# Performance work log

Hardware: AMD Instinct MI355X
Metric: run time of the kernel (lower is better)

The kernel has to match this reference:

```python
import jax, jax.numpy as jnp
import numpy as np

N = 100000      # number of nodes
E = 1600000     # number of (directed) edges, avg degree 16
DIN = 128       # in_features
DOUT = 32       # out_features
SLOPE = 0.2     # leaky relu negative slope


def setup_inputs() -> dict:
    key = jax.random.key(0)
    k1, k2, k3, k4, k5, k6 = jax.random.split(key, 6)
    x = jax.random.normal(k1, (N, DIN), dtype=jnp.float32)
    edge_index = jax.random.randint(k2, (2, E), 0, N, dtype=jnp.int32)
    # W1 (shared with W2 and used as the feature-update matrix W, 'source' mode)
    W1_w = jax.random.normal(k3, (DOUT, DIN), dtype=jnp.float32) / np.float32(np.sqrt(DIN))
    W1_b = jax.random.normal(k4, (DOUT,), dtype=jnp.float32) * 0.01
    a1_w = jax.random.normal(k5, (DOUT,), dtype=jnp.float32) / np.float32(np.sqrt(DOUT))
    a2_w = jax.random.normal(k6, (DOUT,), dtype=jnp.float32) / np.float32(np.sqrt(DOUT))
    return {"x": x, "edge_index": edge_index, "W1_w": W1_w, "W1_b": W1_b,
            "a1_w": a1_w, "a2_w": a2_w}


def reference(x, edge_index, W1_w, W1_b, a1_w, a2_w):
    n = x.shape[0]
    # append self-loops, as in _sparse_attention
    loops = jnp.arange(n, dtype=edge_index.dtype)
    src = jnp.concatenate([edge_index[0], loops])   # rows  (softmax segments)
    dst = jnp.concatenate([edge_index[1], loops])   # cols
    # h = W1(x) (linear, with bias); W2 = W1 (weight sharing), W = W2 ('source')
    h = x @ W1_w.T + W1_b                           # [N, DOUT]
    z = jax.nn.leaky_relu(h, SLOPE)                 # x1 == x2 under weight sharing
    s1 = z @ a1_w                                   # [N] per-node src score
    s2 = z @ a2_w                                   # [N] per-node dst score
    logits = s1[src] + s2[dst]                      # [E+N] per-edge attention logit
    # row-wise (dim=1) sparse softmax == segment softmax over src
    m = jax.ops.segment_max(logits, src, num_segments=n)
    ex = jnp.exp(logits - m[src])
    denom = jax.ops.segment_sum(ex, src, num_segments=n)
    alpha = ex / denom[src]                         # normalized attention per edge
    # sparse-dense matmul: out[i] = sum_{(i,j)} alpha_ij * h[j]
    return jax.ops.segment_sum(alpha[:, None] * h[dst], src, num_segments=n)
```

## Files before the change

kernel.cpp:

```cpp
#include <hip/hip_runtime.h>
#include <hip/hip_fp16.h>

#define DIN 128
#define DOUT 32
#define SLOPE 0.2f

#define BSHIFT 7
#define BNODES 128
#define NBS    1024
#define CAP    3072
#define SRTCAP (CAP + 384)
#define TILE   4096
#define EPB    (TILE / 256)
#define TPW    4

typedef short s16x8 __attribute__((ext_vector_type(8)));
typedef float f32x4 __attribute__((ext_vector_type(4)));

__device__ __forceinline__ short f2bf(float f) {
    unsigned u = __float_as_uint(f);
    return (short)((u + 0x7fffu + ((u >> 16) & 1u)) >> 16);
}
__device__ __forceinline__ float bf2f(short s) {
    return __uint_as_float(((unsigned)(unsigned short)s) << 16);
}

__device__ __forceinline__ void linear_role(
    int wid, int ntiles, int lane, int N,
    const float* __restrict__ x, const float* __restrict__ W,
    const float* __restrict__ b, const float* __restrict__ a2,
    __half* __restrict__ g16, float* __restrict__ es2)
{
    if (wid * TPW >= ntiles) return;
    int m = lane & 15, oct = lane >> 4;

    s16x8 bh[2][4], bl[2][4];
    #pragma unroll
    for (int t = 0; t < 2; ++t) {
        const float* wrow = W + (long)(t * 16 + m) * DIN + oct * 8;
        #pragma unroll
        for (int kc = 0; kc < 4; ++kc) {
            float4 w0 = *(const float4*)(wrow + kc * 32);
            float4 w1 = *(const float4*)(wrow + kc * 32 + 4);
            float wf[8] = {w0.x, w0.y, w0.z, w0.w, w1.x, w1.y, w1.z, w1.w};
            #pragma unroll
            for (int j = 0; j < 8; ++j) {
                short hh = f2bf(wf[j]);
                bh[t][kc][j] = hh;
                bl[t][kc][j] = f2bf(wf[j] - bf2f(hh));
            }
        }
    }

    int c0 = m, c1 = 16 + m;
    float b0 = b[c0], b1 = b[c1], A0 = a2[c0], A1 = a2[c1];

    float4 cxa[4];
    {
        long lrow = (long)(wid * TPW) * 16 + m; if (lrow > N - 1) lrow = N - 1;
        const float* xrow = x + lrow * DIN + oct * 8;
        #pragma unroll
        for (int kc = 0; kc < 2; ++kc) {
            cxa[2 * kc]     = *(const float4*)(xrow + kc * 32);
            cxa[2 * kc + 1] = *(const float4*)(xrow + kc * 32 + 4);
        }
    }

    #pragma unroll 1
    for (int g = 0; g < TPW; ++g) {
        int tile = wid * TPW + g;
        if (tile >= ntiles) break;
        long rowbase = (long)tile * 16;
        long lrow = rowbase + m; if (lrow > N - 1) lrow = N - 1;
        const float* xrow = x + lrow * DIN + oct * 8;

        float4 cxb[4];
        #pragma unroll
        for (int kc = 0; kc < 2; ++kc) {
            cxb[2 * kc]     = *(const float4*)(xrow + (kc + 2) * 32);
            cxb[2 * kc + 1] = *(const float4*)(xrow + (kc + 2) * 32 + 4);
        }

        bool hasnext = (g + 1 < TPW) && (tile + 1 < ntiles);
        float4 nxa[4];
        if (hasnext) {
            long nrow = rowbase + 16 + m; if (nrow > N - 1) nrow = N - 1;
            const float* nx = x + nrow * DIN + oct * 8;
            #pragma unroll
            for (int kc = 0; kc < 2; ++kc) {
                nxa[2 * kc]     = *(const float4*)(nx + kc * 32);
                nxa[2 * kc + 1] = *(const float4*)(nx + kc * 32 + 4);
            }
        }

        f32x4 acc0 = {0.f, 0.f, 0.f, 0.f}, acc1 = {0.f, 0.f, 0.f, 0.f};
        #pragma unroll
        for (int kc = 0; kc < 4; ++kc) {
            float4 x0 = (kc < 2) ? cxa[2 * kc]     : cxb[2 * (kc - 2)];
            float4 x1 = (kc < 2) ? cxa[2 * kc + 1] : cxb[2 * (kc - 2) + 1];
            float xf[8] = {x0.x, x0.y, x0.z, x0.w, x1.x, x1.y, x1.z, x1.w};
            s16x8 ah, al;
            #pragma unroll
            for (int j = 0; j < 8; ++j) {
                short hh = f2bf(xf[j]);
                ah[j] = hh;
                al[j] = f2bf(xf[j] - bf2f(hh));
            }
            acc0 = __builtin_amdgcn_mfma_f32_16x16x32_bf16(al, bh[0][kc], acc0, 0, 0, 0);
            acc0 = __builtin_amdgcn_mfma_f32_16x16x32_bf16(ah, bl[0][kc], acc0, 0, 0, 0);
            acc0 = __builtin_amdgcn_mfma_f32_16x16x32_bf16(ah, bh[0][kc], acc0, 0, 0, 0);
            acc1 = __builtin_amdgcn_mfma_f32_16x16x32_bf16(al, bh[1][kc], acc1, 0, 0, 0);
            acc1 = __builtin_amdgcn_mfma_f32_16x16x32_bf16(ah, bl[1][kc], acc1, 0, 0, 0);
            acc1 = __builtin_amdgcn_mfma_f32_16x16x32_bf16(ah, bh[1][kc], acc1, 0, 0, 0);
        }

        float hv0[4], hv1[4], sp[4];
        #pragma unroll
        for (int i = 0; i < 4; ++i) {
            hv0[i] = acc0[i] + b0;
            hv1[i] = acc1[i] + b1;
            float z0 = hv0[i] > 0.f ? hv0[i] : SLOPE * hv0[i];
            float z1 = hv1[i] > 0.f ? hv1[i] : SLOPE * hv1[i];
            sp[i] = z0 * A0 + z1 * A1;
        }
        #pragma unroll
        for (int off = 1; off <= 8; off <<= 1) {
            #pragma unroll
            for (int i = 0; i < 4; ++i) sp[i] += __shfl_xor(sp[i], off, 64);
        }
        #pragma unroll
        for (int i = 0; i < 4; ++i) {
            long r = rowbase + oct * 4 + i;
            if (r >= N) continue;
            float ev = __expf(sp[i]);
            g16[r * DOUT + c0] = __float2half(ev * hv0[i]);
            g16[r * DOUT + c1] = __float2half(ev * hv1[i]);
            if (m == 0) es2[r] = ev;
        }
        if (hasnext) {
            #pragma unroll
            for (int i = 0; i < 4; ++i) cxa[i] = nxa[i];
        }
    }
}

__global__ __launch_bounds__(256) void gat_fused(
    const float* __restrict__ x, const float* __restrict__ W,
    const float* __restrict__ b, const float* __restrict__ a2,
    const int* __restrict__ src, const int* __restrict__ dst,
    __half* __restrict__ g16, float* __restrict__ es2,
    unsigned* __restrict__ ebuf, int* __restrict__ boffT,
    int N, int E, int ntiles, int nbin, int nbinp)
{
    if ((int)blockIdx.x >= nbin) {
        int wave = threadIdx.x >> 6;
        int wid = (blockIdx.x - nbin) * 4 + wave;
        linear_role(wid, ntiles, threadIdx.x & 63, N, x, W, b, a2, g16, es2);
        return;
    }
    __shared__ int cnt[NBS];
    __shared__ int offs[NBS];
    __shared__ int wsum[4], wbase[4];
    int tid = threadIdx.x;
    long tstart = (long)blockIdx.x * TILE;

    for (int i = tid; i < NBS; i += 256) cnt[i] = 0;
    __syncthreads();

    unsigned rec[EPB];
    int      bq[EPB];
    #pragma unroll
    for (int it = 0; it < EPB; ++it) {
        long e = tstart + it * 256 + tid;
        int s = (e < E) ? src[e] : -1;
        int d = (e < E) ? dst[e] : 0;
        if (s >= 0) {
            int bk = s >> BSHIFT;
            int rv = atomicAdd(&cnt[bk], 1);
            rec[it] = ((unsigned)(s & (BNODES - 1)) << 17) | (unsigned)d;
            bq[it] = (rv < 511) ? ((bk << 9) | rv) : -1;
        } else bq[it] = -1;
    }
    __syncthreads();

    int t4 = tid << 2;
    int c0 = cnt[t4], c1 = cnt[t4 + 1], c2 = cnt[t4 + 2], c3 = cnt[t4 + 3];
    int s4 = c0 + c1 + c2 + c3;
    int v = s4;
    #pragma unroll
    for (int off = 1; off < 64; off <<= 1) {
        int t = __shfl_up(v, off, 64);
        if ((tid & 63) >= off) v += t;
    }
    if ((tid & 63) == 63) wsum[tid >> 6] = v;
    __syncthreads();
    if (tid == 0) {
        int a = 0;
        #pragma unroll
        for (int w = 0; w < 4; ++w) { wbase[w] = a; a += wsum[w]; }
    }
    __syncthreads();
    int base = wbase[tid >> 6] + (v - s4);
    offs[t4]     = base;
    offs[t4 + 1] = base + c0;
    offs[t4 + 2] = base + c0 + c1;
    offs[t4 + 3] = base + c0 + c1 + c2;
    __syncthreads();

    int NBv = (N + BNODES - 1) >> BSHIFT;
    for (int i = tid; i <= NBv; i += 256)
        boffT[(size_t)i * nbinp + blockIdx.x] = offs[i];

    #pragma unroll
    for (int it = 0; it < EPB; ++it) {
        int q = bq[it];
        if (q >= 0) {
            int pos = offs[q >> 9] + (q & 511);
            ebuf[tstart + pos] = rec[it];
        }
    }
}

__global__ __launch_bounds__(512) void gat_aggregate(
    const __half* __restrict__ g16, const float* __restrict__ es2,
    const unsigned* __restrict__ ebuf, const int* __restrict__ boffT,
    float* __restrict__ out, int N, int nbin, int nbinp)
{
    __shared__ unsigned srt[SRTCAP];
    __shared__ unsigned srca[CAP];
    __shared__ int cnt[BNODES];
    __shared__ int basep[BNODES];
    __shared__ int pos2[BNODES];
    __shared__ int wsum[8], wbase[8], totsh;
    int tid = threadIdx.x;

    int nwg = gridDim.x;
    int xcd = blockIdx.x & 7;
    int q = nwg >> 3, rr = nwg & 7;
    int bk = (xcd < rr ? xcd * (q + 1) : rr * (q + 1) + (xcd - rr) * q)
           + ((int)blockIdx.x >> 3);

    if (tid < BNODES) { cnt[tid] = 0; pos2[tid] = 0; }

    int rstart = 0, rlen = 0;
    if (tid < nbin) {
        rstart = boffT[(size_t)bk * nbinp + tid];
        rlen   = boffT[(size_t)(bk + 1) * nbinp + tid] - rstart;
    }
    int v = rlen;
    #pragma unroll
    for (int off = 1; off < 64; off <<= 1) {
        int t = __shfl_up(v, off, 64);
        if ((tid & 63) >= off) v += t;
    }
    if ((tid & 63) == 63) wsum[tid >> 6] = v;
    __syncthreads();
    if (tid == 0) {
        int a = 0;
        #pragma unroll
        for (int w = 0; w < 8; ++w) { wbase[w] = a; a += wsum[w]; }
        totsh = a;
    }
    __syncthreads();
    int dest = wbase[tid >> 6] + (v - rlen);
    int lim = CAP - dest; if (lim < 0) lim = 0;
    if (rlen > lim) rlen = lim;
    {
        unsigned abase = (unsigned)tid * TILE + (unsigned)rstart;
        for (int j = 0; j < rlen; ++j)
            srca[dest + j] = abase + (unsigned)j;
    }
    __syncthreads();
    int cntb = totsh; if (cntb > CAP) cntb = CAP;

    unsigned held[6];
    #pragma unroll
    for (int k = 0; k < 6; ++k) {
        int r = tid + (k << 9);
        held[k] = 0xFFFFFFFFu;
        if (r < cntb) held[k] = ebuf[(size_t)srca[r]];
    }
    #pragma unroll
    for (int k = 0; k < 6; ++k) {
        unsigned u = held[k];
        if (u != 0xFFFFFFFFu) atomicAdd(&cnt[u >> 17], 1);
    }
    __syncthreads();

    if (tid < 64) {
        int a = cnt[2 * tid], b2 = cnt[2 * tid + 1];
        int pa = (a + 3) & ~3, pb = (b2 + 3) & ~3;
        int s = pa + pb;
        int vv = s;
        #pragma unroll
        for (int off = 1; off < 64; off <<= 1) {
            int t = __shfl_up(vv, off, 64);
            if (tid >= off) vv += t;
        }
        int excl = vv - s;
        basep[2 * tid]     = excl;
        basep[2 * tid + 1] = excl + pa;
    }
    __syncthreads();

    #pragma unroll
    for (int k = 0; k < 6; ++k) {
        unsigned u = held[k];
        if (u != 0xFFFFFFFFu) {
            int sl = (int)(u >> 17);
            int p = basep[sl] + atomicAdd(&pos2[sl], 1);
            srt[p] = u & 0x1FFFFu;
        }
    }
    __syncthreads();

    int unit = tid >> 5, col = tid & 31;
    int lane64 = tid & 63;
    for (int sl = unit; sl < BNODES; sl += 16) {
        long node = (long)bk * BNODES + sl;
        if (node >= N) break;
        float acc = __half2float(g16[node * DOUT + col]);
        float selfe = es2[node];
        float dpart = 0.f;
        int e = basep[sl], e_end = basep[sl] + cnt[sl];

        while (e + 8 <= e_end) {
            uint4 q0 = *(const uint4*)&srt[e];
            uint4 q1 = *(const uint4*)&srt[e + 4];
            float evp = 0.f;
            if (col < 8) evp = es2[srt[e + col]];
            int dn[8] = {(int)q0.x, (int)q0.y, (int)q0.z, (int)q0.w,
                         (int)q1.x, (int)q1.y, (int)q1.z, (int)q1.w};
            unsigned short gv[8];
            #pragma unroll
            for (int j = 0; j < 8; ++j)
                gv[j] = *(const unsigned short*)&g16[(long)dn[j] * DOUT + col];
            dpart += evp;
            #pragma unroll
            for (int j = 0; j < 8; ++j)
                acc += __half2float(*(const __half*)&gv[j]);
            e += 8;
        }
        while (e + 4 <= e_end) {
            uint4 q0 = *(const uint4*)&srt[e];
            float evp = 0.f;
            if (col < 4) evp = es2[srt[e + col]];
            int dn[4] = {(int)q0.x, (int)q0.y, (int)q0.z, (int)q0.w};
            unsigned short gv[4];
            #pragma unroll
            for (int j = 0; j < 4; ++j)
                gv[j] = *(const unsigned short*)&g16[(long)dn[j] * DOUT + col];
            dpart += evp;
            #pragma unroll
            for (int j = 0; j < 4; ++j)
                acc += __half2float(*(const __half*)&gv[j]);
            e += 4;
        }
        for (; e < e_end; ++e) {
            int dn = (int)srt[e];
            acc += __half2float(g16[(long)dn * DOUT + col]);
            if (col == 0) dpart += es2[dn];
        }
        #pragma unroll
        for (int off = 1; off < 8; off <<= 1)
            dpart += __shfl_xor(dpart, off, 64);
        float dtot = __shfl(dpart, lane64 & 32, 64);
        out[node * DOUT + col] = acc / (selfe + dtot);
    }
}

extern "C" void kernel_launch(void* const* d_in, const int* in_sizes, int n_in,
                              void* d_out, int out_size, void* d_ws, size_t ws_size,
                              hipStream_t stream)
{
    const float* x  = (const float*)d_in[0];
    const int*   ei = (const int*)d_in[1];
    const float* W  = (const float*)d_in[2];
    const float* b  = (const float*)d_in[3];
    const float* a2 = (const float*)d_in[5];
    float* out = (float*)d_out;

    int N = in_sizes[0] / DIN;
    int E = in_sizes[1] / 2;
    const int* src = ei;
    const int* dst = ei + E;

    int NB = (N + BNODES - 1) >> BSHIFT;
    int nbin = (E + TILE - 1) / TILE;
    int nbinp = (nbin + 7) & ~7;

    char* ws = (char*)d_ws;
    __half*   g16   = (__half*)ws;  ws += (size_t)N * DOUT * sizeof(__half);
    float*    es2   = (float*)ws;   ws += (size_t)N * sizeof(float);
    int*      boffT = (int*)ws;     ws += (size_t)(NB + 1) * nbinp * sizeof(int);
    unsigned* ebuf  = (unsigned*)ws; ws += (size_t)nbin * TILE * sizeof(unsigned);

    int ntiles = (N + 15) / 16;
    int nwaves = (ntiles + TPW - 1) / TPW;
    int nlin   = (nwaves + 3) / 4;

    gat_fused    <<<nbin + nlin, 256, 0, stream>>>(x, W, b, a2, src, dst,
                                                   g16, es2, ebuf, boffT,
                                                   N, E, ntiles, nbin, nbinp);
    gat_aggregate<<<NB, 512, 0, stream>>>(g16, es2, ebuf, boffT, out, N,
                                          nbin, nbinp);
}
```

Baseline: 155.1 us.

## Stage split bf16 weights in LDS and give each linear wave one tile

Linear-role blocks now convert W into bf16 hi/lo halves once per block and store them in a swizzled 16KB shared buffer, so waves no longer convert W in registers themselves. Each wave processes a single 16-row tile instead of four, which removes the x prefetch pipeline and roughly quadruples the number of linear blocks. Binning blocks now reuse the same shared buffer for their counters. This adds a block-wide conversion and barrier for every small block, and the larger shared allocation applies to binning blocks too, which may reduce occupancy.

```diff
diff --git a/kernel.cpp b/kernel.cpp
--- a/kernel.cpp
+++ b/kernel.cpp
@@ -12,7 +12,8 @@
 #define SRTCAP (CAP + 384)
 #define TILE   4096
 #define EPB    (TILE / 256)
-#define TPW    4
+
+#define FSMEM  16384
 
 typedef short s16x8 __attribute__((ext_vector_type(8)));
 typedef float f32x4 __attribute__((ext_vector_type(4)));
@@ -25,122 +26,77 @@
     return __uint_as_float(((unsigned)(unsigned short)s) << 16);
 }
 
-__device__ __forceinline__ void linear_role(
-    int wid, int ntiles, int lane, int N,
-    const float* __restrict__ x, const float* __restrict__ W,
+__device__ __forceinline__ void linear_tile(
+    int tile, int ntiles, int lane, int N,
+    const unsigned short* __restrict__ Whi, const unsigned short* __restrict__ Wlo,
+    const float* __restrict__ x,
     const float* __restrict__ b, const float* __restrict__ a2,
     __half* __restrict__ g16, float* __restrict__ es2)
 {
-    if (wid * TPW >= ntiles) return;
+    if (tile >= ntiles) return;
     int m = lane & 15, oct = lane >> 4;
 
     s16x8 bh[2][4], bl[2][4];
     #pragma unroll
     for (int t = 0; t < 2; ++t) {
-        const float* wrow = W + (long)(t * 16 + m) * DIN + oct * 8;
+        int row = t * 16 + m;
         #pragma unroll
         for (int kc = 0; kc < 4; ++kc) {
-            float4 w0 = *(const float4*)(wrow + kc * 32);
-            float4 w1 = *(const float4*)(wrow + kc * 32 + 4);
-            float wf[8] = {w0.x, w0.y, w0.z, w0.w, w1.x, w1.y, w1.z, w1.w};
-            #pragma unroll
-            for (int j = 0; j < 8; ++j) {
-                short hh = f2bf(wf[j]);
-                bh[t][kc][j] = hh;
-                bl[t][kc][j] = f2bf(wf[j] - bf2f(hh));
-            }
+            int sch = (kc * 4 + oct) ^ m;
+            bh[t][kc] = *(const s16x8*)((const char*)Whi + row * 256 + sch * 16);
+            bl[t][kc] = *(const s16x8*)((const char*)Wlo + row * 256 + sch * 16);
         }
     }
 
     int c0 = m, c1 = 16 + m;
     float b0 = b[c0], b1 = b[c1], A0 = a2[c0], A1 = a2[c1];
 
-    float4 cxa[4];
-    {
-        long lrow = (long)(wid * TPW) * 16 + m; if (lrow > N - 1) lrow = N - 1;
-        const float* xrow = x + lrow * DIN + oct * 8;
-        #pragma unroll
-        for (int kc = 0; kc < 2; ++kc) {
-            cxa[2 * kc]     = *(const float4*)(xrow + kc * 32);
-            cxa[2 * kc + 1] = *(const float4*)(xrow + kc * 32 + 4);
-        }
-    }
-
-    #pragma unroll 1
-    for (int g = 0; g < TPW; ++g) {
-        int tile = wid * TPW + g;
-        if (tile >= ntiles) break;
-        long rowbase = (long)tile * 16;
-        long lrow = rowbase + m; if (lrow > N - 1) lrow = N - 1;
-        const float* xrow = x + lrow * DIN + oct * 8;
-
-        float4 cxb[4];
-        #pragma unroll
-        for (int kc = 0; kc < 2; ++kc) {
-            cxb[2 * kc]     = *(const float4*)(xrow + (kc + 2) * 32);
-            cxb[2 * kc + 1] = *(const float4*)(xrow + (kc + 2) * 32 + 4);
-        }
-
-        bool hasnext = (g + 1 < TPW) && (tile + 1 < ntiles);
-        float4 nxa[4];
-        if (hasnext) {
-            long nrow = rowbase + 16 + m; if (nrow > N - 1) nrow = N - 1;
-            const float* nx = x + nrow * DIN + oct * 8;
-            #pragma unroll
-            for (int kc = 0; kc < 2; ++kc) {
-                nxa[2 * kc]     = *(const float4*)(nx + kc * 32);
-                nxa[2 * kc + 1] = *(const float4*)(nx + kc * 32 + 4);
-            }
-        }
-
-        f32x4 acc0 = {0.f, 0.f, 0.f, 0.f}, acc1 = {0.f, 0.f, 0.f, 0.f};
-        #pragma unroll
-        for (int kc = 0; kc < 4; ++kc) {
-            float4 x0 = (kc < 2) ? cxa[2 * kc]     : cxb[2 * (kc - 2)];
-            float4 x1 = (kc < 2) ? cxa[2 * kc + 1] : cxb[2 * (kc - 2) + 1];
-            float xf[8] = {x0.x, x0.y, x0.z, x0.w, x1.x, x1.y, x1.z, x1.w};
-            s16x8 ah, al;
-            #pragma unroll
-            for (int j = 0; j < 8; ++j) {
-                short hh = f2bf(xf[j]);
-                ah[j] = hh;
-                al[j] = f2bf(xf[j] - bf2f(hh));
-            }
-            acc0 = __builtin_amdgcn_mfma_f32_16x16x32_bf16(al, bh[0][kc], acc0, 0, 0, 0);
-            acc0 = __builtin_amdgcn_mfma_f32_16x16x32_bf16(ah, bl[0][kc], acc0, 0, 0, 0);
-            acc0 = __builtin_amdgcn_mfma_f32_16x16x32_bf16(ah, bh[0][kc], acc0, 0, 0, 0);
-            acc1 = __builtin_amdgcn_mfma_f32_16x16x32_bf16(al, bh[1][kc], acc1, 0, 0, 0);
-            acc1 = __builtin_amdgcn_mfma_f32_16x16x32_bf16(ah, bl[1][kc], acc1, 0, 0, 0);
-            acc1 = __builtin_amdgcn_mfma_f32_16x16x32_bf16(ah, bh[1][kc], acc1, 0, 0, 0);
-        }
-
-        float hv0[4], hv1[4], sp[4];
-        #pragma unroll
-        for (int i = 0; i < 4; ++i) {
-            hv0[i] = acc0[i] + b0;
-            hv1[i] = acc1[i] + b1;
-            float z0 = hv0[i] > 0.f ? hv0[i] : SLOPE * hv0[i];
-            float z1 = hv1[i] > 0.f ? hv1[i] : SLOPE * hv1[i];
-            sp[i] = z0 * A0 + z1 * A1;
-        }
-        #pragma unroll
-        for (int off = 1; off <= 8; off <<= 1) {
-            #pragma unroll
-            for (int i = 0; i < 4; ++i) sp[i] += __shfl_xor(sp[i], off, 64);
-        }
-        #pragma unroll
-        for (int i = 0; i < 4; ++i) {
-            long r = rowbase + oct * 4 + i;
-            if (r >= N) continue;
-            float ev = __expf(sp[i]);
-            g16[r * DOUT + c0] = __float2half(ev * hv0[i]);
-            g16[r * DOUT + c1] = __float2half(ev * hv1[i]);
-            if (m == 0) es2[r] = ev;
-        }
-        if (hasnext) {
-            #pragma unroll
-            for (int i = 0; i < 4; ++i) cxa[i] = nxa[i];
-        }
+    long rowbase = (long)tile * 16;
+    long lrow = rowbase + m; if (lrow > N - 1) lrow = N - 1;
+    const float* xrow = x + lrow * DIN + oct * 8;
+    f32x4 acc0 = {0.f, 0.f, 0.f, 0.f}, acc1 = {0.f, 0.f, 0.f, 0.f};
+    #pragma unroll
+    for (int kc = 0; kc < 4; ++kc) {
+        float4 x0 = *(const float4*)(xrow + kc * 32);
+        float4 x1 = *(const float4*)(xrow + kc * 32 + 4);
+        float xf[8] = {x0.x, x0.y, x0.z, x0.w, x1.x, x1.y, x1.z, x1.w};
+        s16x8 ah, al;
+        #pragma unroll
+        for (int j = 0; j < 8; ++j) {
+            short hh = f2bf(xf[j]);
+            ah[j] = hh;
+            al[j] = f2bf(xf[j] - bf2f(hh));
+        }
+        acc0 = __builtin_amdgcn_mfma_f32_16x16x32_bf16(al, bh[0][kc], acc0, 0, 0, 0);
+        acc0 = __builtin_amdgcn_mfma_f32_16x16x32_bf16(ah, bl[0][kc], acc0, 0, 0, 0);
+        acc0 = __builtin_amdgcn_mfma_f32_16x16x32_bf16(ah, bh[0][kc], acc0, 0, 0, 0);
+        acc1 = __builtin_amdgcn_mfma_f32_16x16x32_bf16(al, bh[1][kc], acc1, 0, 0, 0);
+        acc1 = __builtin_amdgcn_mfma_f32_16x16x32_bf16(ah, bl[1][kc], acc1, 0, 0, 0);
+        acc1 = __builtin_amdgcn_mfma_f32_16x16x32_bf16(ah, bh[1][kc], acc1, 0, 0, 0);
+    }
+
+    float hv0[4], hv1[4], sp[4];
+    #pragma unroll
+    for (int i = 0; i < 4; ++i) {
+        hv0[i] = acc0[i] + b0;
+        hv1[i] = acc1[i] + b1;
+        float z0 = hv0[i] > 0.f ? hv0[i] : SLOPE * hv0[i];
+        float z1 = hv1[i] > 0.f ? hv1[i] : SLOPE * hv1[i];
+        sp[i] = z0 * A0 + z1 * A1;
+    }
+    #pragma unroll
+    for (int off = 1; off <= 8; off <<= 1) {
+        #pragma unroll
+        for (int i = 0; i < 4; ++i) sp[i] += __shfl_xor(sp[i], off, 64);
+    }
+    #pragma unroll
+    for (int i = 0; i < 4; ++i) {
+        long r = rowbase + oct * 4 + i;
+        if (r >= N) continue;
+        float ev = __expf(sp[i]);
+        g16[r * DOUT + c0] = __float2half(ev * hv0[i]);
+        g16[r * DOUT + c1] = __float2half(ev * hv1[i]);
+        if (m == 0) es2[r] = ev;
     }
 }
 
@@ -152,16 +108,40 @@
     unsigned* __restrict__ ebuf, int* __restrict__ boffT,
     int N, int E, int ntiles, int nbin, int nbinp)
 {
+    __shared__ __align__(16) unsigned char smem[FSMEM];
+    int tid = threadIdx.x;
+
     if ((int)blockIdx.x >= nbin) {
-        int wave = threadIdx.x >> 6;
-        int wid = (blockIdx.x - nbin) * 4 + wave;
-        linear_role(wid, ntiles, threadIdx.x & 63, N, x, W, b, a2, g16, es2);
+        unsigned short* Whi = (unsigned short*)smem;
+        unsigned short* Wlo = (unsigned short*)(smem + 8192);
+        for (int c = tid; c < 512; c += 256) {
+            int row = c >> 4, ch = c & 15;
+            const float* wsrc = W + (long)row * DIN + ch * 8;
+            float4 a  = *(const float4*)wsrc;
+            float4 b4 = *(const float4*)(wsrc + 4);
+            float wf[8] = {a.x, a.y, a.z, a.w, b4.x, b4.y, b4.z, b4.w};
+            s16x8 hi, lo;
+            #pragma unroll
+            for (int j = 0; j < 8; ++j) {
+                short hh = f2bf(wf[j]);
+                hi[j] = hh;
+                lo[j] = f2bf(wf[j] - bf2f(hh));
+            }
+            int sch = ch ^ (row & 15);
+            *(s16x8*)((char*)Whi + row * 256 + sch * 16) = hi;
+            *(s16x8*)((char*)Wlo + row * 256 + sch * 16) = lo;
+        }
+        __syncthreads();
+        int wave = tid >> 6;
+        int tile = ((int)blockIdx.x - nbin) * 4 + wave;
+        linear_tile(tile, ntiles, tid & 63, N, Whi, Wlo, x, b, a2, g16, es2);
         return;
     }
-    __shared__ int cnt[NBS];
-    __shared__ int offs[NBS];
-    __shared__ int wsum[4], wbase[4];
-    int tid = threadIdx.x;
+
+    int* cnt   = (int*)smem;
+    int* offs  = (int*)(smem + 4096);
+    int* wsum  = (int*)(smem + 8192);
+    int* wbase = (int*)(smem + 8208);
     long tstart = (long)blockIdx.x * TILE;
 
     for (int i = tid; i < NBS; i += 256) cnt[i] = 0;
@@ -396,8 +376,7 @@
     unsigned* ebuf  = (unsigned*)ws; ws += (size_t)nbin * TILE * sizeof(unsigned);
 
     int ntiles = (N + 15) / 16;
-    int nwaves = (ntiles + TPW - 1) / TPW;
-    int nlin   = (nwaves + 3) / 4;
+    int nlin   = (ntiles + 3) / 4;
 
     gat_fused    <<<nbin + nlin, 256, 0, stream>>>(x, W, b, a2, src, dst,
                                                    g16, es2, ebuf, boffT,
```

Measured after the change: 148.8 us (median of 2 runs). 1.04x faster.
